# Kernel optimization log

Hardware: AMD Instinct MI355X
Metric: run time of the kernel (lower is better)

The kernel has to match this reference:

```python
import jax, jax.numpy as jnp
import numpy as np

N_NODES = 100000
N_EDGES = 1600000
LN_EPS = 1e-5
CLAMP = 1.8


def setup_inputs() -> dict:
    key = jax.random.key(0)
    ks = jax.random.split(key, 12)
    feats = [100, 64, 64, 47]
    inp = {
        "x": jax.random.normal(ks[0], (N_NODES, feats[0]), dtype=jnp.float32),
        "adj_vals": jax.random.uniform(ks[1], (N_EDGES,), dtype=jnp.float32),
        "adj_row": jax.random.randint(ks[2], (N_EDGES,), 0, N_NODES),
        "adj_col": jax.random.randint(ks[3], (N_EDGES,), 0, N_NODES),
        "ln_gamma": jnp.ones((feats[0],), dtype=jnp.float32),
        "ln_beta": jnp.zeros((feats[0],), dtype=jnp.float32),
    }
    for i in range(3):
        fi, fo = feats[i], feats[i + 1]
        bound = 1.0 / np.sqrt(fi)
        inp[f"W{i+1}"] = jax.random.uniform(ks[4 + 2 * i], (fi, fo), minval=-bound, maxval=bound, dtype=jnp.float32)
        inp[f"b{i+1}"] = jax.random.uniform(ks[5 + 2 * i], (fo,), minval=-bound, maxval=bound, dtype=jnp.float32)
    return inp


def _spmm(vals, row, col, x):
    # out[i] = sum_{e: row[e]==i} vals[e] * x[col[e]]
    gathered = vals[:, None] * x[col]  # [E, D]
    return jax.ops.segment_sum(gathered, row, num_segments=N_NODES)


def reference(x, adj_vals, adj_row, adj_col, ln_gamma, ln_beta, W1, b1, W2, b2, W3, b3):
    # clamp to [-1.8, 1.8]: relu(x+1.8)-1.8 then 1.8-relu(1.8-x)
    x = jnp.clip(x, -CLAMP, CLAMP)
    # LayerNorm over last dim (100)
    mu = jnp.mean(x, axis=-1, keepdims=True)
    var = jnp.mean(jnp.square(x - mu), axis=-1, keepdims=True)
    x = (x - mu) * jax.lax.rsqrt(var + LN_EPS) * ln_gamma + ln_beta
    # GCN layers: Linear -> spmm -> (elu except last); dropout=0 => identity
    x = jax.nn.elu(_spmm(adj_vals, adj_row, adj_col, x @ W1 + b1))
    x = jax.nn.elu(_spmm(adj_vals, adj_row, adj_col, x @ W2 + b2))
    x = _spmm(adj_vals, adj_row, adj_col, x @ W3 + b3)
    return x
```

## Files before the change

kernel.cpp:

```cpp
#include <hip/hip_runtime.h>
#include <cstdint>
#include <cstddef>

#define N_NODES_C 100000
#define N_EDGES_C 1600000
#define LN_EPS_C 1e-5f
#define CLAMP_C 1.8f
#define SC_BLOCKS 1024
#define LN_BLOCKS 1024

typedef unsigned short ushort_t;

__device__ __forceinline__ float readlane_f(float v, int l) {
  return __uint_as_float(__builtin_amdgcn_readlane(__float_as_uint(v), l));
}

__device__ __forceinline__ float wave_sum(float v) {
#pragma unroll
  for (int off = 32; off > 0; off >>= 1) v += __shfl_xor(v, off, 64);
  return v;
}

__device__ __forceinline__ ushort_t f2bf(float f) {
  unsigned u = __float_as_uint(f);
  unsigned r = (u + 0x7fffu + ((u >> 16) & 1u)) >> 16;
  return (ushort_t)r;
}
__device__ __forceinline__ float bf2f(ushort_t u) {
  return __uint_as_float((unsigned)u << 16);
}

__global__ __launch_bounds__(256) void hist_kernel(const int* __restrict__ row,
                                                   int* __restrict__ counts) {
  int tid = blockIdx.x * blockDim.x + threadIdx.x;
  int nt = gridDim.x * blockDim.x;
  int r[8];
#pragma unroll
  for (int k = 0; k < 8; ++k) {
    int e = tid + k * nt;
    r[k] = (e < N_EDGES_C) ? row[e] : -1;
  }
#pragma unroll
  for (int k = 0; k < 8; ++k)
    if (r[k] >= 0) atomicAdd(&counts[r[k]], 1);
}

__global__ void scan1_kernel(const int* __restrict__ counts, int* __restrict__ rowstart,
                             int* __restrict__ bsums) {
  __shared__ int lds[256];
  int t = threadIdx.x;
  int base = blockIdx.x * 1024 + t * 4;
  int c0 = (base + 0 < N_NODES_C) ? counts[base + 0] : 0;
  int c1 = (base + 1 < N_NODES_C) ? counts[base + 1] : 0;
  int c2 = (base + 2 < N_NODES_C) ? counts[base + 2] : 0;
  int c3 = (base + 3 < N_NODES_C) ? counts[base + 3] : 0;
  int s = c0 + c1 + c2 + c3;
  lds[t] = s;
  __syncthreads();
#pragma unroll
  for (int off = 1; off < 256; off <<= 1) {
    int v = (t >= off) ? lds[t - off] : 0;
    __syncthreads();
    lds[t] += v;
    __syncthreads();
  }
  int incl = lds[t];
  int excl = incl - s;
  if (t == 255) bsums[blockIdx.x] = incl;
  if (base + 0 < N_NODES_C) rowstart[base + 0] = excl;
  excl += c0;
  if (base + 1 < N_NODES_C) rowstart[base + 1] = excl;
  excl += c1;
  if (base + 2 < N_NODES_C) rowstart[base + 2] = excl;
  excl += c2;
  if (base + 3 < N_NODES_C) rowstart[base + 3] = excl;
}

__global__ void scan2_kernel(int* __restrict__ bsums, int nb) {
  __shared__ int lds[128];
  int t = threadIdx.x;
  int v = (t < nb) ? bsums[t] : 0;
  lds[t] = v;
  __syncthreads();
#pragma unroll
  for (int off = 1; off < 128; off <<= 1) {
    int u = (t >= off) ? lds[t - off] : 0;
    __syncthreads();
    lds[t] += u;
    __syncthreads();
  }
  if (t < nb) bsums[t] = lds[t] - v;
}

__global__ void scan3_kernel(int* __restrict__ rowstart, int* __restrict__ cursor,
                             const int* __restrict__ bsums) {
  int add = bsums[blockIdx.x];
  int base = blockIdx.x * 1024 + threadIdx.x * 4;
#pragma unroll
  for (int i = 0; i < 4; ++i)
    if (base + i < N_NODES_C) {
      int v = rowstart[base + i] + add;
      rowstart[base + i] = v;
      cursor[base + i] = v;
    }
}

__global__ __launch_bounds__(256) void scatter_ln_kernel(
    const int* __restrict__ row, const int* __restrict__ col,
    const float* __restrict__ vals, int* __restrict__ cursor,
    int2* __restrict__ edges_s,
    const float* __restrict__ x, const float* __restrict__ gamma,
    const float* __restrict__ beta, const float* __restrict__ W1,
    const float* __restrict__ b1, ushort_t* __restrict__ y) {
  if ((blockIdx.x & 1) == 0) {
    int tid = (blockIdx.x >> 1) * 256 + threadIdx.x;
    const int nt = SC_BLOCKS * 256;
    int r[8], c[8], p[8];
    float v[8];
#pragma unroll
    for (int k = 0; k < 8; ++k) {
      int e = tid + k * nt;
      bool in = e < N_EDGES_C;
      r[k] = in ? row[e] : 0;
      c[k] = in ? col[e] : 0;
      v[k] = in ? vals[e] : 0.f;
    }
#pragma unroll
    for (int k = 0; k < 8; ++k) {
      int e = tid + k * nt;
      if (e < N_EDGES_C) p[k] = atomicAdd(&cursor[r[k]], 1);
    }
#pragma unroll
    for (int k = 0; k < 8; ++k) {
      int e = tid + k * nt;
      if (e < N_EDGES_C) edges_s[p[k]] = make_int2(c[k], __float_as_int(v[k]));
    }
  } else {
    int lane = threadIdx.x & 63;
    int wid = (blockIdx.x >> 1) * 4 + (threadIdx.x >> 6);
    const int nw = LN_BLOCKS * 4;
    float bias = b1[lane];
    float g0 = gamma[lane];
    float be0 = beta[lane];
    float g1 = (lane < 36) ? gamma[64 + lane] : 0.f;
    float be1 = (lane < 36) ? beta[64 + lane] : 0.f;
    for (int n = wid; n < N_NODES_C; n += nw) {
      const float* xr = x + (size_t)n * 100;
      float x0 = xr[lane];
      float x1 = (lane < 36) ? xr[64 + lane] : 0.f;
      x0 = fminf(fmaxf(x0, -CLAMP_C), CLAMP_C);
      x1 = fminf(fmaxf(x1, -CLAMP_C), CLAMP_C);
      float mu = wave_sum(x0 + x1) * 0.01f;
      float d0 = x0 - mu;
      float d1 = (lane < 36) ? (x1 - mu) : 0.f;
      float var = wave_sum(d0 * d0 + d1 * d1) * 0.01f;
      float inv = rsqrtf(var + LN_EPS_C);
      float xn0 = d0 * inv * g0 + be0;
      float xn1 = d1 * inv * g1 + be1;
      float acc = bias;
#pragma unroll
      for (int k = 0; k < 64; ++k) acc = fmaf(readlane_f(xn0, k), W1[k * 64 + lane], acc);
#pragma unroll
      for (int k = 0; k < 36; ++k) acc = fmaf(readlane_f(xn1, k), W1[(64 + k) * 64 + lane], acc);
      y[(size_t)n * 64 + lane] = f2bf(acc);
    }
  }
}

template <int DOUT>
__global__ __launch_bounds__(256) void spmm_elu_gemm_kernel(
    const int* __restrict__ rowstart, const int* __restrict__ counts,
    const int2* __restrict__ edges_s, const ushort_t* __restrict__ yb,
    const float* __restrict__ W, const float* __restrict__ b,
    ushort_t* __restrict__ out) {
  int lane = threadIdx.x & 63;
  int wid = blockIdx.x * (blockDim.x >> 6) + (threadIdx.x >> 6);
  int nw = gridDim.x * (blockDim.x >> 6);
  float w[64];
#pragma unroll
  for (int k = 0; k < 64; ++k) w[k] = (lane < DOUT) ? W[k * DOUT + lane] : 0.f;
  float bias = (lane < DOUT) ? b[lane] : 0.f;
  for (int n = wid; n < N_NODES_C; n += nw) {
    int start = rowstart[n];
    int cnt = counts[n];
    float a[8];
#pragma unroll
    for (int u = 0; u < 8; ++u) a[u] = 0.f;
    for (int base = 0; base < cnt; base += 64) {
      int m = cnt - base;
      if (m > 64) m = 64;
      int2 ev = make_int2(0, 0);
      if (lane < m) ev = edges_s[start + base + lane];
      int mr = (m + 15) & ~15;
      for (int j = 0; j < mr; j += 16) {
        float g[16];
#pragma unroll
        for (int u = 0; u < 16; ++u)
          g[u] = bf2f(yb[(size_t)__builtin_amdgcn_readlane(ev.x, j + u) * 64 + lane]);
#pragma unroll
        for (int u = 0; u < 16; ++u)
          a[u & 7] = fmaf(
              __uint_as_float(__builtin_amdgcn_readlane((unsigned)ev.y, j + u)), g[u],
              a[u & 7]);
      }
    }
    float acc = ((a[0] + a[1]) + (a[2] + a[3])) + ((a[4] + a[5]) + (a[6] + a[7]));
    float xe = (acc > 0.f) ? acc : expm1f(acc);
    float o = bias;
#pragma unroll
    for (int k = 0; k < 64; ++k) o = fmaf(readlane_f(xe, k), w[k], o);
    if (lane < DOUT) out[(size_t)n * 64 + lane] = f2bf(o);
  }
}

__global__ __launch_bounds__(256) void spmm_final_kernel(
    const int* __restrict__ rowstart, const int* __restrict__ counts,
    const int2* __restrict__ edges_s, const ushort_t* __restrict__ yb,
    float* __restrict__ out) {
  int lane = threadIdx.x & 63;
  int wid = blockIdx.x * (blockDim.x >> 6) + (threadIdx.x >> 6);
  int nw = gridDim.x * (blockDim.x >> 6);
  int lmask = (lane < 47) ? lane : 46;
  for (int n = wid; n < N_NODES_C; n += nw) {
    int start = rowstart[n];
    int cnt = counts[n];
    float a[8];
#pragma unroll
    for (int u = 0; u < 8; ++u) a[u] = 0.f;
    for (int base = 0; base < cnt; base += 64) {
      int m = cnt - base;
      if (m > 64) m = 64;
      int2 ev = make_int2(0, 0);
      if (lane < m) ev = edges_s[start + base + lane];
      int mr = (m + 15) & ~15;
      for (int j = 0; j < mr; j += 16) {
        float g[16];
#pragma unroll
        for (int u = 0; u < 16; ++u)
          g[u] = bf2f(yb[(size_t)__builtin_amdgcn_readlane(ev.x, j + u) * 64 + lmask]);
#pragma unroll
        for (int u = 0; u < 16; ++u)
          a[u & 7] = fmaf(
              __uint_as_float(__builtin_amdgcn_readlane((unsigned)ev.y, j + u)), g[u],
              a[u & 7]);
      }
    }
    float acc = ((a[0] + a[1]) + (a[2] + a[3])) + ((a[4] + a[5]) + (a[6] + a[7]));
    if (lane < 47) out[(size_t)n * 47 + lane] = acc;
  }
}

extern "C" void kernel_launch(void* const* d_in, const int* in_sizes, int n_in,
                              void* d_out, int out_size, void* d_ws, size_t ws_size,
                              hipStream_t stream) {
  const float* x = (const float*)d_in[0];
  const float* adj_vals = (const float*)d_in[1];
  const int* adj_row = (const int*)d_in[2];
  const int* adj_col = (const int*)d_in[3];
  const float* gamma = (const float*)d_in[4];
  const float* beta = (const float*)d_in[5];
  const float* W1 = (const float*)d_in[6];
  const float* b1 = (const float*)d_in[7];
  const float* W2 = (const float*)d_in[8];
  const float* b2 = (const float*)d_in[9];
  const float* W3 = (const float*)d_in[10];
  const float* b3 = (const float*)d_in[11];
  float* out = (float*)d_out;

  char* ws = (char*)d_ws;
  size_t off = 0;
  auto alloc = [&](size_t bytes) -> void* {
    void* p = ws + off;
    off += (bytes + 255) & ~(size_t)255;
    return p;
  };
  ushort_t* bufA = (ushort_t*)alloc(sizeof(ushort_t) * (size_t)N_NODES_C * 64);
  ushort_t* bufB = (ushort_t*)alloc(sizeof(ushort_t) * (size_t)N_NODES_C * 64);
  int* counts = (int*)alloc(sizeof(int) * N_NODES_C);
  int* cursor = (int*)alloc(sizeof(int) * N_NODES_C);
  int* rowstart = (int*)alloc(sizeof(int) * N_NODES_C);
  int* bsums = (int*)alloc(sizeof(int) * 256);
  int2* edges_s = (int2*)alloc(sizeof(int2) * N_EDGES_C);

  hipMemsetAsync(counts, 0, sizeof(int) * N_NODES_C, stream);

  hist_kernel<<<782, 256, 0, stream>>>(adj_row, counts);
  int nb = (N_NODES_C + 1023) / 1024;
  scan1_kernel<<<nb, 256, 0, stream>>>(counts, rowstart, bsums);
  scan2_kernel<<<1, 128, 0, stream>>>(bsums, nb);
  scan3_kernel<<<nb, 256, 0, stream>>>(rowstart, cursor, bsums);

  scatter_ln_kernel<<<SC_BLOCKS + LN_BLOCKS, 256, 0, stream>>>(
      adj_row, adj_col, adj_vals, cursor, edges_s, x, gamma, beta, W1, b1, bufA);

  spmm_elu_gemm_kernel<64><<<2048, 256, 0, stream>>>(rowstart, counts, edges_s, bufA,
                                                     W2, b2, bufB);
  spmm_elu_gemm_kernel<47><<<2048, 256, 0, stream>>>(rowstart, counts, edges_s, bufB,
                                                     W3, b3, bufA);
  spmm_final_kernel<<<2048, 256, 0, stream>>>(rowstart, counts, edges_s, bufA, out);
}
```

Measured before the change: 405.8 us.

## Drop per-lane weight registers, prefetch next row bounds, raise occupancy and grid

The SpMM+ELU+GEMM kernels stop caching 64 weight values per lane in registers and instead load W from memory (cache) inside the epilogue, freeing registers so that launch_bounds(256,8) can target higher occupancy. All three SpMM kernels now software-prefetch the next row's start and count while processing the current row, and grids double to 4096 blocks. The aim is more waves in flight to hide gather latency, at the cost of 64 extra weight loads per node in the epilogue.

```diff
diff --git a/kernel.cpp b/kernel.cpp
--- a/kernel.cpp
+++ b/kernel.cpp
@@ -168,7 +168,7 @@
 }
 
 template <int DOUT>
-__global__ __launch_bounds__(256) void spmm_elu_gemm_kernel(
+__global__ __launch_bounds__(256, 8) void spmm_elu_gemm_kernel(
     const int* __restrict__ rowstart, const int* __restrict__ counts,
     const int2* __restrict__ edges_s, const ushort_t* __restrict__ yb,
     const float* __restrict__ W, const float* __restrict__ b,
@@ -176,13 +176,14 @@
   int lane = threadIdx.x & 63;
   int wid = blockIdx.x * (blockDim.x >> 6) + (threadIdx.x >> 6);
   int nw = gridDim.x * (blockDim.x >> 6);
-  float w[64];
-#pragma unroll
-  for (int k = 0; k < 64; ++k) w[k] = (lane < DOUT) ? W[k * DOUT + lane] : 0.f;
   float bias = (lane < DOUT) ? b[lane] : 0.f;
-  for (int n = wid; n < N_NODES_C; n += nw) {
-    int start = rowstart[n];
-    int cnt = counts[n];
+  int n = wid;
+  int start = (n < N_NODES_C) ? rowstart[n] : 0;
+  int cnt = (n < N_NODES_C) ? counts[n] : 0;
+  for (; n < N_NODES_C;) {
+    int n2 = n + nw;
+    int s2 = (n2 < N_NODES_C) ? rowstart[n2] : 0;
+    int c2 = (n2 < N_NODES_C) ? counts[n2] : 0;
     float a[8];
 #pragma unroll
     for (int u = 0; u < 8; ++u) a[u] = 0.f;
@@ -208,12 +209,16 @@
     float xe = (acc > 0.f) ? acc : expm1f(acc);
     float o = bias;
 #pragma unroll
-    for (int k = 0; k < 64; ++k) o = fmaf(readlane_f(xe, k), w[k], o);
+    for (int k = 0; k < 64; ++k)
+      o = fmaf(readlane_f(xe, k), (lane < DOUT) ? W[k * DOUT + lane] : 0.f, o);
     if (lane < DOUT) out[(size_t)n * 64 + lane] = f2bf(o);
-  }
-}
-
-__global__ __launch_bounds__(256) void spmm_final_kernel(
+    n = n2;
+    start = s2;
+    cnt = c2;
+  }
+}
+
+__global__ __launch_bounds__(256, 8) void spmm_final_kernel(
     const int* __restrict__ rowstart, const int* __restrict__ counts,
     const int2* __restrict__ edges_s, const ushort_t* __restrict__ yb,
     float* __restrict__ out) {
@@ -221,9 +226,13 @@
   int wid = blockIdx.x * (blockDim.x >> 6) + (threadIdx.x >> 6);
   int nw = gridDim.x * (blockDim.x >> 6);
   int lmask = (lane < 47) ? lane : 46;
-  for (int n = wid; n < N_NODES_C; n += nw) {
-    int start = rowstart[n];
-    int cnt = counts[n];
+  int n = wid;
+  int start = (n < N_NODES_C) ? rowstart[n] : 0;
+  int cnt = (n < N_NODES_C) ? counts[n] : 0;
+  for (; n < N_NODES_C;) {
+    int n2 = n + nw;
+    int s2 = (n2 < N_NODES_C) ? rowstart[n2] : 0;
+    int c2 = (n2 < N_NODES_C) ? counts[n2] : 0;
     float a[8];
 #pragma unroll
     for (int u = 0; u < 8; ++u) a[u] = 0.f;
@@ -247,6 +256,9 @@
     }
     float acc = ((a[0] + a[1]) + (a[2] + a[3])) + ((a[4] + a[5]) + (a[6] + a[7]));
     if (lane < 47) out[(size_t)n * 47 + lane] = acc;
+    n = n2;
+    start = s2;
+    cnt = c2;
   }
 }
 
@@ -293,9 +305,9 @@
   scatter_ln_kernel<<<SC_BLOCKS + LN_BLOCKS, 256, 0, stream>>>(
       adj_row, adj_col, adj_vals, cursor, edges_s, x, gamma, beta, W1, b1, bufA);
 
-  spmm_elu_gemm_kernel<64><<<2048, 256, 0, stream>>>(rowstart, counts, edges_s, bufA,
+  spmm_elu_gemm_kernel<64><<<4096, 256, 0, stream>>>(rowstart, counts, edges_s, bufA,
                                                      W2, b2, bufB);
-  spmm_elu_gemm_kernel<47><<<2048, 256, 0, stream>>>(rowstart, counts, edges_s, bufB,
+  spmm_elu_gemm_kernel<47><<<4096, 256, 0, stream>>>(rowstart, counts, edges_s, bufB,
                                                      W3, b3, bufA);
-  spmm_final_kernel<<<2048, 256, 0, stream>>>(rowstart, counts, edges_s, bufA, out);
-}
+  spmm_final_kernel<<<4096, 256, 0, stream>>>(rowstart, counts, edges_s, bufA, out);
+}
```

New measurement: 1.083 ms. 2.67x slower.

## Partition CSR scatter by XCC so each die owns a row range

Applied to the files above, without the earlier changes.

The edge scatter is split into 8 row partitions. Each scatter block reads its XCC id from a hardware register and starts with the partition for its own die. Blocks pull edge slices from a per-partition atomic work pool, and each pass re-reads every row index while only handling edges whose row falls in the current partition. The goal is to keep cursor atomics and edges_s writes local to one XCC's L2 and cut cross-die traffic. The cost is reading the row array about 8 times plus extra block-level synchronisation for work stealing.

```diff
diff --git a/kernel.cpp b/kernel.cpp
--- a/kernel.cpp
+++ b/kernel.cpp
@@ -8,6 +8,10 @@
 #define CLAMP_C 1.8f
 #define SC_BLOCKS 1024
 #define LN_BLOCKS 1024
+#define ROWS_PER_PART 12500
+#define SLICES 128
+#define SLICE_SZ 12500
+#define XCC_ID_GETREG 14356
 
 typedef unsigned short ushort_t;
 
@@ -108,32 +112,57 @@
 __global__ __launch_bounds__(256) void scatter_ln_kernel(
     const int* __restrict__ row, const int* __restrict__ col,
     const float* __restrict__ vals, int* __restrict__ cursor,
-    int2* __restrict__ edges_s,
+    int* __restrict__ pool, int2* __restrict__ edges_s,
     const float* __restrict__ x, const float* __restrict__ gamma,
     const float* __restrict__ beta, const float* __restrict__ W1,
     const float* __restrict__ b1, ushort_t* __restrict__ y) {
+  __shared__ int s_chunk;
   if ((blockIdx.x & 1) == 0) {
-    int tid = (blockIdx.x >> 1) * 256 + threadIdx.x;
-    const int nt = SC_BLOCKS * 256;
-    int r[8], c[8], p[8];
-    float v[8];
-#pragma unroll
-    for (int k = 0; k < 8; ++k) {
-      int e = tid + k * nt;
-      bool in = e < N_EDGES_C;
-      r[k] = in ? row[e] : 0;
-      c[k] = in ? col[e] : 0;
-      v[k] = in ? vals[e] : 0.f;
-    }
-#pragma unroll
-    for (int k = 0; k < 8; ++k) {
-      int e = tid + k * nt;
-      if (e < N_EDGES_C) p[k] = atomicAdd(&cursor[r[k]], 1);
-    }
-#pragma unroll
-    for (int k = 0; k < 8; ++k) {
-      int e = tid + k * nt;
-      if (e < N_EDGES_C) edges_s[p[k]] = make_int2(c[k], __float_as_int(v[k]));
+    int my = __builtin_amdgcn_s_getreg(XCC_ID_GETREG) & 7;
+    for (int d = 0; d < 8; ++d) {
+      int xp = (my + d) & 7;
+      int rlo = xp * ROWS_PER_PART;
+      while (true) {
+        __syncthreads();
+        if (threadIdx.x == 0) s_chunk = atomicAdd(&pool[xp], 1);
+        __syncthreads();
+        int s = s_chunk;
+        if (s >= SLICES) break;
+        int e0 = s * SLICE_SZ;
+        int e1 = e0 + SLICE_SZ;
+        if (e1 > N_EDGES_C) e1 = N_EDGES_C;
+        for (int base = e0; base < e1; base += 2048) {
+          int rr[8], cc[8], pp[8];
+          float vv[8];
+          bool own[8];
+#pragma unroll
+          for (int k = 0; k < 8; ++k) {
+            int e = base + (int)threadIdx.x + k * 256;
+            rr[k] = (e < e1) ? row[e] : -1;
+          }
+#pragma unroll
+          for (int k = 0; k < 8; ++k)
+            own[k] = ((unsigned)(rr[k] - rlo) < (unsigned)ROWS_PER_PART);
+#pragma unroll
+          for (int k = 0; k < 8; ++k) {
+            int e = base + (int)threadIdx.x + k * 256;
+            cc[k] = 0;
+            vv[k] = 0.f;
+            if (own[k]) {
+              cc[k] = col[e];
+              vv[k] = vals[e];
+            }
+          }
+#pragma unroll
+          for (int k = 0; k < 8; ++k) {
+            pp[k] = 0;
+            if (own[k]) pp[k] = atomicAdd(&cursor[rr[k]], 1);
+          }
+#pragma unroll
+          for (int k = 0; k < 8; ++k)
+            if (own[k]) edges_s[pp[k]] = make_int2(cc[k], __float_as_int(vv[k]));
+        }
+      }
     }
   } else {
     int lane = threadIdx.x & 63;
@@ -280,9 +309,11 @@
   int* cursor = (int*)alloc(sizeof(int) * N_NODES_C);
   int* rowstart = (int*)alloc(sizeof(int) * N_NODES_C);
   int* bsums = (int*)alloc(sizeof(int) * 256);
+  int* pool = (int*)alloc(sizeof(int) * 8);
   int2* edges_s = (int2*)alloc(sizeof(int2) * N_EDGES_C);
 
   hipMemsetAsync(counts, 0, sizeof(int) * N_NODES_C, stream);
+  hipMemsetAsync(pool, 0, sizeof(int) * 8, stream);
 
   hist_kernel<<<782, 256, 0, stream>>>(adj_row, counts);
   int nb = (N_NODES_C + 1023) / 1024;
@@ -291,7 +322,7 @@
   scan3_kernel<<<nb, 256, 0, stream>>>(rowstart, cursor, bsums);
 
   scatter_ln_kernel<<<SC_BLOCKS + LN_BLOCKS, 256, 0, stream>>>(
-      adj_row, adj_col, adj_vals, cursor, edges_s, x, gamma, beta, W1, b1, bufA);
+      adj_row, adj_col, adj_vals, cursor, pool, edges_s, x, gamma, beta, W1, b1, bufA);
 
   spmm_elu_gemm_kernel<64><<<2048, 256, 0, stream>>>(rowstart, counts, edges_s, bufA,
                                                      W2, b2, bufB);
```

New measurement: 491.4 us. 21.1% more time.

## Two-pass bucketed CSR scatter via per-1024-row bin partitioning

Applied to the files above, without the earlier changes.

Replaces the direct random scatter of edges into CSR order with two passes. A partition kernel first groups each 4096-edge chunk by 1024-row bin in shared memory and writes it contiguously into a staging buffer. A bin-scatter kernel then places each bin's edges using per-row cursor atomics, so writes stay within a localized window. This aims at better write locality and cache behavior for the scatter, at the cost of an extra kernel launch, extra staging traffic and only 98 blocks for the scatter phase.

```diff
diff --git a/kernel.cpp b/kernel.cpp
--- a/kernel.cpp
+++ b/kernel.cpp
@@ -6,8 +6,11 @@
 #define N_EDGES_C 1600000
 #define LN_EPS_C 1e-5f
 #define CLAMP_C 1.8f
-#define SC_BLOCKS 1024
 #define LN_BLOCKS 1024
+#define BINS 98
+#define CHUNK 4096
+#define EPT 16
+#define NCHUNK 391
 
 typedef unsigned short ushort_t;
 
@@ -93,51 +96,122 @@
 }
 
 __global__ void scan3_kernel(int* __restrict__ rowstart, int* __restrict__ cursor,
-                             const int* __restrict__ bsums) {
+                             int* __restrict__ bincur, const int* __restrict__ bsums) {
   int add = bsums[blockIdx.x];
   int base = blockIdx.x * 1024 + threadIdx.x * 4;
 #pragma unroll
-  for (int i = 0; i < 4; ++i)
-    if (base + i < N_NODES_C) {
-      int v = rowstart[base + i] + add;
-      rowstart[base + i] = v;
-      cursor[base + i] = v;
-    }
-}
-
-__global__ __launch_bounds__(256) void scatter_ln_kernel(
+  for (int i = 0; i < 4; ++i) {
+    int rI = base + i;
+    if (rI < N_NODES_C) {
+      int v = rowstart[rI] + add;
+      rowstart[rI] = v;
+      cursor[rI] = v;
+      if ((rI & 1023) == 0) bincur[rI >> 10] = v;
+    }
+  }
+}
+
+__global__ __launch_bounds__(256) void partition_kernel(
     const int* __restrict__ row, const int* __restrict__ col,
-    const float* __restrict__ vals, int* __restrict__ cursor,
+    const float* __restrict__ vals, int* __restrict__ bincur,
+    int2* __restrict__ stage_cv, ushort_t* __restrict__ stage_rlo) {
+  __shared__ int hist[128];
+  __shared__ int scanarr[128];
+  __shared__ int cnt2[128];
+  __shared__ int basearr[128];
+  __shared__ int2 s_cv[CHUNK];
+  __shared__ ushort_t s_rlo[CHUNK];
+  __shared__ unsigned char s_bin[CHUNK];
+  int t = threadIdx.x;
+  int e0 = blockIdx.x * CHUNK;
+  if (t < 128) {
+    hist[t] = 0;
+    cnt2[t] = 0;
+    basearr[t] = 0;
+  }
+  __syncthreads();
+  int rr[EPT], cc[EPT], bn[EPT];
+  float vv[EPT];
+#pragma unroll
+  for (int k = 0; k < EPT; ++k) {
+    int e = e0 + t + k * 256;
+    bool valid = e < N_EDGES_C;
+    rr[k] = valid ? row[e] : -1;
+    cc[k] = valid ? col[e] : 0;
+    vv[k] = valid ? vals[e] : 0.f;
+  }
+#pragma unroll
+  for (int k = 0; k < EPT; ++k) {
+    bn[k] = (rr[k] >= 0) ? (rr[k] >> 10) : -1;
+    if (bn[k] >= 0) atomicAdd(&hist[bn[k]], 1);
+  }
+  __syncthreads();
+  if (t < 128) scanarr[t] = hist[t];
+  __syncthreads();
+#pragma unroll
+  for (int off = 1; off < 128; off <<= 1) {
+    int u = 0;
+    if (t < 128 && t >= off) u = scanarr[t - off];
+    __syncthreads();
+    if (t < 128) scanarr[t] += u;
+    __syncthreads();
+  }
+  if (t < BINS && hist[t] > 0) basearr[t] = atomicAdd(&bincur[t], hist[t]);
+#pragma unroll
+  for (int k = 0; k < EPT; ++k) {
+    if (bn[k] >= 0) {
+      int lstart = scanarr[bn[k]] - hist[bn[k]];
+      int slot = lstart + atomicAdd(&cnt2[bn[k]], 1);
+      s_cv[slot] = make_int2(cc[k], __float_as_int(vv[k]));
+      s_rlo[slot] = (ushort_t)(rr[k] & 1023);
+      s_bin[slot] = (unsigned char)bn[k];
+    }
+  }
+  __syncthreads();
+  int totv = scanarr[127];
+  for (int s = t; s < totv; s += 256) {
+    int b = s_bin[s];
+    int lstart = scanarr[b] - hist[b];
+    int g = basearr[b] + (s - lstart);
+    stage_cv[g] = s_cv[s];
+    stage_rlo[g] = s_rlo[s];
+  }
+}
+
+__global__ __launch_bounds__(256) void binscatter_ln_kernel(
+    const int* __restrict__ rowstart, const int2* __restrict__ stage_cv,
+    const ushort_t* __restrict__ stage_rlo, int* __restrict__ cursor,
     int2* __restrict__ edges_s,
     const float* __restrict__ x, const float* __restrict__ gamma,
     const float* __restrict__ beta, const float* __restrict__ W1,
     const float* __restrict__ b1, ushort_t* __restrict__ y) {
-  if ((blockIdx.x & 1) == 0) {
-    int tid = (blockIdx.x >> 1) * 256 + threadIdx.x;
-    const int nt = SC_BLOCKS * 256;
-    int r[8], c[8], p[8];
-    float v[8];
-#pragma unroll
-    for (int k = 0; k < 8; ++k) {
-      int e = tid + k * nt;
-      bool in = e < N_EDGES_C;
-      r[k] = in ? row[e] : 0;
-      c[k] = in ? col[e] : 0;
-      v[k] = in ? vals[e] : 0.f;
-    }
-#pragma unroll
-    for (int k = 0; k < 8; ++k) {
-      int e = tid + k * nt;
-      if (e < N_EDGES_C) p[k] = atomicAdd(&cursor[r[k]], 1);
-    }
-#pragma unroll
-    for (int k = 0; k < 8; ++k) {
-      int e = tid + k * nt;
-      if (e < N_EDGES_C) edges_s[p[k]] = make_int2(c[k], __float_as_int(v[k]));
+  if (blockIdx.x < BINS) {
+    int b = blockIdx.x;
+    int t = threadIdx.x;
+    int lo = rowstart[b << 10];
+    int hi = (b == BINS - 1) ? N_EDGES_C : rowstart[(b + 1) << 10];
+    int rbase = b << 10;
+    for (int i0 = lo; i0 < hi; i0 += 2048) {
+      int2 cv[8];
+      int rn[8], p[8];
+      bool in[8];
+#pragma unroll
+      for (int k = 0; k < 8; ++k) {
+        int i = i0 + t + k * 256;
+        in[k] = i < hi;
+        cv[k] = in[k] ? stage_cv[i] : make_int2(0, 0);
+        rn[k] = in[k] ? (rbase | (int)stage_rlo[i]) : 0;
+      }
+#pragma unroll
+      for (int k = 0; k < 8; ++k)
+        if (in[k]) p[k] = atomicAdd(&cursor[rn[k]], 1);
+#pragma unroll
+      for (int k = 0; k < 8; ++k)
+        if (in[k]) edges_s[p[k]] = cv[k];
     }
   } else {
     int lane = threadIdx.x & 63;
-    int wid = (blockIdx.x >> 1) * 4 + (threadIdx.x >> 6);
+    int wid = ((int)blockIdx.x - BINS) * 4 + (threadIdx.x >> 6);
     const int nw = LN_BLOCKS * 4;
     float bias = b1[lane];
     float g0 = gamma[lane];
@@ -280,7 +354,10 @@
   int* cursor = (int*)alloc(sizeof(int) * N_NODES_C);
   int* rowstart = (int*)alloc(sizeof(int) * N_NODES_C);
   int* bsums = (int*)alloc(sizeof(int) * 256);
+  int* bincur = (int*)alloc(sizeof(int) * 128);
   int2* edges_s = (int2*)alloc(sizeof(int2) * N_EDGES_C);
+  int2* stage_cv = (int2*)alloc(sizeof(int2) * N_EDGES_C);
+  ushort_t* stage_rlo = (ushort_t*)alloc(sizeof(ushort_t) * N_EDGES_C);
 
   hipMemsetAsync(counts, 0, sizeof(int) * N_NODES_C, stream);
 
@@ -288,10 +365,12 @@
   int nb = (N_NODES_C + 1023) / 1024;
   scan1_kernel<<<nb, 256, 0, stream>>>(counts, rowstart, bsums);
   scan2_kernel<<<1, 128, 0, stream>>>(bsums, nb);
-  scan3_kernel<<<nb, 256, 0, stream>>>(rowstart, cursor, bsums);
-
-  scatter_ln_kernel<<<SC_BLOCKS + LN_BLOCKS, 256, 0, stream>>>(
-      adj_row, adj_col, adj_vals, cursor, edges_s, x, gamma, beta, W1, b1, bufA);
+  scan3_kernel<<<nb, 256, 0, stream>>>(rowstart, cursor, bincur, bsums);
+
+  partition_kernel<<<NCHUNK, 256, 0, stream>>>(adj_row, adj_col, adj_vals, bincur,
+                                               stage_cv, stage_rlo);
+  binscatter_ln_kernel<<<BINS + LN_BLOCKS, 256, 0, stream>>>(
+      rowstart, stage_cv, stage_rlo, cursor, edges_s, x, gamma, beta, W1, b1, bufA);
 
   spmm_elu_gemm_kernel<64><<<2048, 256, 0, stream>>>(rowstart, counts, edges_s, bufA,
                                                      W2, b2, bufB);
```

Result: faster. 394.5 us (median of 2 runs) (-2.8%).
